# Kernel optimization log

Measured on AMD Instinct MI355X. Metric: run time of the kernel, lower is better.

## Reference

```python
import jax, jax.numpy as jnp
import numpy as np

B, C, H, W = 8, 128, 64, 64
D_STATE = 16
D_CONV = 4
EXPAND = 1.25
D_INNER = int(EXPAND * C)        # 160
DT_RANK = int(np.ceil(C / 16))   # 8


def setup_inputs() -> dict:
    key = jax.random.key(0)
    ks = jax.random.split(key, 10)
    f = lambda k, s, sc=0.02: jax.random.normal(k, s, dtype=jnp.float32) * sc
    return {
        "x": jax.random.normal(ks[0], (B, C, H, W), dtype=jnp.float32),
        "ln_g": jnp.ones((C,), jnp.float32),
        "ln_b": jnp.zeros((C,), jnp.float32),
        "in_proj_w": f(ks[1], (2 * D_INNER, C)),
        "conv_w": f(ks[2], (D_INNER, 1, D_CONV)),            # depthwise causal conv kernel
        "conv_b": jnp.zeros((D_INNER,), jnp.float32),
        "x_proj_w": f(ks[3], (DT_RANK + 2 * D_STATE, D_INNER)),
        "dt_proj_w": f(ks[4], (D_INNER, DT_RANK), 0.1),
        "dt_proj_b": f(ks[5], (D_INNER,), 0.1),
        # S4-style init: A_log = log(1..d_state) per inner channel (frozen in torch module)
        "A_log": jnp.log(jnp.tile(jnp.arange(1, D_STATE + 1, dtype=jnp.float32), (D_INNER, 1))),
        "D_param": jnp.ones((D_INNER,), jnp.float32),
        "out_proj_w": f(ks[6], (C, D_INNER)),
        "fuse_w": f(ks[7], (C, 2 * C)),                      # 1x1 conv == per-token matmul
        "scale": jnp.ones((1,), jnp.float32) * 0.1,
    }


def _layernorm(x, g, b, eps=1e-5):
    m = x.mean(-1, keepdims=True)
    v = x.var(-1, keepdims=True)
    return (x - m) * jax.lax.rsqrt(v + eps) * g + b


def _mamba(seq, in_proj_w, conv_w, conv_b, x_proj_w, dt_proj_w, dt_proj_b,
           A_log, D_param, out_proj_w):
    # seq: (B, L, C)
    Bsz, L, _ = seq.shape
    xz = jnp.einsum('blc,ec->ble', seq, in_proj_w)           # (B, L, 2*d_inner)
    xm, z = jnp.split(xz, 2, axis=-1)
    # depthwise causal conv over L, truncated to L (padding = d_conv-1 on the left)
    xc = jax.lax.conv_general_dilated(
        xm.transpose(0, 2, 1), conv_w, (1,), [(D_CONV - 1, 0)],
        feature_group_count=D_INNER, dimension_numbers=('NCH', 'OIH', 'NCH'))
    xm = jax.nn.silu((xc + conv_b[None, :, None]).transpose(0, 2, 1))  # (B, L, d_inner)
    x_dbl = jnp.einsum('bld,ed->ble', xm, x_proj_w)
    dt = x_dbl[..., :DT_RANK]
    Bm = x_dbl[..., DT_RANK:DT_RANK + D_STATE]               # (B, L, d_state)
    Cm = x_dbl[..., DT_RANK + D_STATE:]                      # (B, L, d_state)
    dt = jax.nn.softplus(jnp.einsum('blr,dr->bld', dt, dt_proj_w) + dt_proj_b)
    A = -jnp.exp(A_log)                                      # (d_inner, d_state)

    def step(h, inp):
        dt_t, B_t, C_t, x_t = inp                            # (B,d) (B,n) (B,n) (B,d)
        dA = jnp.exp(dt_t[:, :, None] * A)                   # (B, d_inner, d_state)
        h = dA * h + (dt_t * x_t)[:, :, None] * B_t[:, None, :]
        y = jnp.einsum('bdn,bn->bd', h, C_t)
        return h, y

    h0 = jnp.zeros((Bsz, D_INNER, D_STATE), dtype=seq.dtype)
    xs = (dt.transpose(1, 0, 2), Bm.transpose(1, 0, 2),
          Cm.transpose(1, 0, 2), xm.transpose(1, 0, 2))
    _, ys = jax.lax.scan(step, h0, xs)                       # ys: (L, B, d_inner)
    y = ys.transpose(1, 0, 2) + xm * D_param
    y = y * jax.nn.silu(z)
    return jnp.einsum('bld,cd->blc', y, out_proj_w)          # (B, L, C)


def reference(x, ln_g, ln_b, in_proj_w, conv_w, conv_b, x_proj_w, dt_proj_w,
              dt_proj_b, A_log, D_param, out_proj_w, fuse_w, scale):
    Bsz, Ch, Hh, Ww = x.shape
    seq = x.reshape(Bsz, Ch, Hh * Ww).transpose(0, 2, 1)     # (B, L, C) raster order
    seq_n = _layernorm(seq, ln_g, ln_b)                      # LN is per-token: commutes with flip
    args = (in_proj_w, conv_w, conv_b, x_proj_w, dt_proj_w, dt_proj_b,
            A_log, D_param, out_proj_w)
    y0 = _mamba(seq_n, *args)                                # forward raster scan
    y1 = _mamba(seq_n[:, ::-1, :], *args)[:, ::-1, :]        # reversed raster scan
    fused = jnp.einsum('blk,ck->blc', jnp.concatenate([y0, y1], axis=-1), fuse_w)
    out = seq + scale * fused                                # residual + learned scale
    return out.transpose(0, 2, 1).reshape(Bsz, Ch, Hh, Ww)
```

## Files before the change

kernel.cpp:

```cpp
#include <hip/hip_runtime.h>
#include <math.h>

#define LSEQ   4096
#define BATCH  8
#define CDIM   128
#define DIN    160
#define DSTATE 16
#define DTRANK 8
#define BLROWS (BATCH*LSEQ)
#define NCHUNK 256
#define TCH    16
#define SUBC   16
#define NSEG   16

typedef __attribute__((ext_vector_type(8))) short short8;
typedef __attribute__((ext_vector_type(8))) __bf16 bf16x8;
typedef __attribute__((ext_vector_type(4))) float float4v;

__device__ __forceinline__ float4v mfma_bf16(short8 a, short8 b, float4v c) {
  return __builtin_amdgcn_mfma_f32_16x16x32_bf16(
      __builtin_bit_cast(bf16x8, a), __builtin_bit_cast(bf16x8, b), c, 0, 0, 0);
}

__device__ __forceinline__ unsigned short f2bf(float f) {
  union { float f; unsigned u; } v; v.f = f;
  unsigned r = v.u + 0x7FFF + ((v.u >> 16) & 1);
  return (unsigned short)(r >> 16);
}
__device__ __forceinline__ float bf2f(unsigned short h) {
  union { unsigned u; float f; } v; v.u = ((unsigned)h) << 16;
  return v.f;
}

__global__ void prep_weights(const float* __restrict__ inpw, const float* __restrict__ xpw,
                             const float* __restrict__ fuse_w, const float* __restrict__ out_proj_w,
                             unsigned short* __restrict__ inpw_bf, unsigned short* __restrict__ xpw_bf,
                             unsigned short* __restrict__ W01) {
  int i = blockIdx.x * 256 + threadIdx.x;
  if (i < 320 * 128) inpw_bf[i] = f2bf(inpw[i]);
  if (i < 40 * 160)  xpw_bf[i]  = f2bf(xpw[i]);
  if (i < CDIM * DIN) {
    int d = i % DIN, c = i / DIN;
    float a0 = 0.f, a1 = 0.f;
    for (int k = 0; k < CDIM; ++k) {
      float o = out_proj_w[k * DIN + d];
      a0 += fuse_w[c * 256 + k] * o;
      a1 += fuse_w[c * 256 + 128 + k] * o;
    }
    W01[c * DIN + d] = f2bf(a0);
    W01[CDIM * DIN + c * DIN + d] = f2bf(a1);
  }
}

__global__ void ln_transpose_kernel(const float* __restrict__ x,
                                    const float* __restrict__ g,
                                    const float* __restrict__ bb,
                                    unsigned short* __restrict__ seqn) {
  __shared__ float sA[128 * 65];
  __shared__ float psum[2 * 256];
  __shared__ float mrs[2 * 64];
  int l0 = blockIdx.x * 64;
  int b  = blockIdx.y;
  int t  = threadIdx.x;
  int lsub = t & 63, crow = t >> 6;
  const float* xb = x + (size_t)b * CDIM * LSEQ;
  for (int it = 0; it < 32; ++it) {
    int c = crow + it * 4;
    sA[c * 65 + lsub] = xb[(size_t)c * LSEQ + l0 + lsub];
  }
  __syncthreads();
  float s = 0.f, ss = 0.f;
  for (int j = 0; j < 32; ++j) {
    int c = crow * 32 + j;
    float v = sA[c * 65 + lsub];
    s += v; ss += v * v;
  }
  psum[crow * 64 + lsub] = s;
  psum[256 + crow * 64 + lsub] = ss;
  __syncthreads();
  if (t < 64) {
    float su = 0.f, sq = 0.f;
    for (int p = 0; p < 4; ++p) { su += psum[p * 64 + t]; sq += psum[256 + p * 64 + t]; }
    float m = su * (1.f / 128.f);
    float var = sq * (1.f / 128.f) - m * m;
    mrs[t] = m;
    mrs[64 + t] = rsqrtf(var + 1e-5f);
  }
  __syncthreads();
  int c = t & 127, half = t >> 7;
  float gc = g[c], bc = bb[c];
  for (int it = 0; it < 32; ++it) {
    int l = it * 2 + half;
    float v = (sA[c * 65 + l] - mrs[l]) * mrs[64 + l] * gc + bc;
    seqn[((size_t)(b * LSEQ + l0 + l)) * CDIM + c] = f2bf(v);
  }
}

template<int K, bool MASKN, bool BF16OUT>
__global__ __launch_bounds__(256)
void gemm_mfma(const unsigned short* __restrict__ A0, const unsigned short* __restrict__ A1,
               const unsigned short* __restrict__ W,
               void* __restrict__ C0, void* __restrict__ C1, int N) {
  constexpr int LSTR = K + 8;
  __shared__ __align__(16) unsigned short As[64 * LSTR];
  __shared__ __align__(16) unsigned short Ws[64 * LSTR];
  const unsigned short* A = blockIdx.z ? A1 : A0;
  void* Cp = blockIdx.z ? C1 : C0;
  int m0 = blockIdx.x * 64;
  int n0 = blockIdx.y * 64;
  int t = threadIdx.x;
  constexpr int CH = 64 * K / 8;
  for (int c = t; c < CH; c += 256) {
    int row = c / (K / 8);
    int col = (c % (K / 8)) * 8;
    *(short8*)&As[row * LSTR + col] = *(const short8*)&A[(size_t)(m0 + row) * K + col];
    short8 wv = {};
    int nr = n0 + row;
    if (!MASKN || nr < N) wv = *(const short8*)&W[(size_t)nr * K + col];
    *(short8*)&Ws[row * LSTR + col] = wv;
  }
  __syncthreads();
  int lane = t & 63;
  int w = t >> 6;
  int l15 = lane & 15, quad = lane >> 4;
  float4v acc[4] = {};
#pragma unroll
  for (int kk = 0; kk < K; kk += 32) {
    short8 bfrag = *(const short8*)&Ws[(w * 16 + l15) * LSTR + kk + quad * 8];
#pragma unroll
    for (int i = 0; i < 4; ++i) {
      short8 afrag = *(const short8*)&As[(i * 16 + l15) * LSTR + kk + quad * 8];
      acc[i] = mfma_bf16(afrag, bfrag, acc[i]);
    }
  }
  int col = n0 + w * 16 + l15;
  if (MASKN && col >= N) return;
#pragma unroll
  for (int i = 0; i < 4; ++i)
#pragma unroll
    for (int r = 0; r < 4; ++r) {
      int row = m0 + i * 16 + quad * 4 + r;
      if (BF16OUT) ((unsigned short*)Cp)[(size_t)row * N + col] = f2bf(acc[i][r]);
      else         ((float*)Cp)[(size_t)row * N + col] = acc[i][r];
    }
}

__global__ void conv_silu_kernel(const unsigned short* __restrict__ xz,
                                 const float* __restrict__ cw,
                                 const float* __restrict__ cb,
                                 unsigned short* __restrict__ xm0,
                                 unsigned short* __restrict__ xm1,
                                 _Float16* __restrict__ szp) {
  int idx = blockIdx.x * 256 + threadIdx.x;
  int dir = blockIdx.y;
  if (idx >= BLROWS * 80) return;
  int dp = idx % 80;
  int bl = idx / 80;
  int l = bl % LSEQ, b = bl / LSEQ;
  int d = dp * 2;
  float w0[4], w1[4];
#pragma unroll
  for (int k = 0; k < 4; ++k) { w0[k] = cw[d * 4 + k]; w1[k] = cw[d * 4 + 4 + k]; }
  float a0 = cb[d], a1 = cb[d + 1];
  const unsigned short* base = xz + ((size_t)b * LSEQ) * 320 + d;
  if (dir == 0) {
#pragma unroll
    for (int k = 0; k < 4; ++k) {
      int lp = l - 3 + k;
      if (lp >= 0) {
        unsigned v = *(const unsigned*)&base[(size_t)lp * 320];
        a0 += w0[k] * bf2f((unsigned short)v);
        a1 += w1[k] * bf2f((unsigned short)(v >> 16));
      }
    }
  } else {
#pragma unroll
    for (int k = 0; k < 4; ++k) {
      int lp = l + 3 - k;
      if (lp < LSEQ) {
        unsigned v = *(const unsigned*)&base[(size_t)lp * 320];
        a0 += w0[k] * bf2f((unsigned short)v);
        a1 += w1[k] * bf2f((unsigned short)(v >> 16));
      }
    }
  }
  float s0 = a0 / (1.f + __expf(-a0));
  float s1 = a1 / (1.f + __expf(-a1));
  unsigned outv = (unsigned)f2bf(s0) | ((unsigned)f2bf(s1) << 16);
  unsigned short* xm = dir ? xm1 : xm0;
  *(unsigned*)&xm[(size_t)bl * DIN + d] = outv;
  if (dir == 0) {
    unsigned zv = *(const unsigned*)&xz[(size_t)bl * 320 + 160 + d];
    float z0 = bf2f((unsigned short)zv), z1 = bf2f((unsigned short)(zv >> 16));
    float g0 = z0 / (1.f + __expf(-z0));
    float g1 = z1 / (1.f + __expf(-z1));
    unsigned short h0 = __builtin_bit_cast(unsigned short, (_Float16)g0);
    unsigned short h1 = __builtin_bit_cast(unsigned short, (_Float16)g1);
    *(unsigned*)&szp[(size_t)bl * DIN + d] = (unsigned)h0 | ((unsigned)h1 << 16);
  }
}

__device__ __forceinline__ void decay_powers(float r1, float* dA) {
  float r2 = r1 * r1;
  float r4 = r2 * r2;
  float r8 = r4 * r4;
  dA[0] = r1;       dA[1] = r2;       dA[2] = r2 * r1;  dA[3] = r4;
  dA[4] = r4 * r1;  dA[5] = r4 * r2;  dA[6] = r4 * dA[2]; dA[7] = r8;
  dA[8] = r8 * r1;  dA[9] = r8 * r2;  dA[10] = r8 * dA[2]; dA[11] = r8 * r4;
  dA[12] = r8 * dA[4]; dA[13] = r8 * dA[5]; dA[14] = r8 * dA[6]; dA[15] = r8 * r8;
}

__global__ __launch_bounds__(192, 6)
void scan_passA(const float* __restrict__ xdbl0, const float* __restrict__ xdbl1,
                const unsigned short* __restrict__ xm0v, const unsigned short* __restrict__ xm1v,
                const float* __restrict__ dt_w, const float* __restrict__ dt_b,
                const float* __restrict__ Dp,
                float* __restrict__ Q, float* __restrict__ dtsum,
                unsigned* __restrict__ yr0, unsigned* __restrict__ yr1) {
  __shared__ __align__(16) float sx[TCH * 40];
  __shared__ __align__(16) unsigned short sxm[TCH * DIN];
  int chunk = blockIdx.x, b = blockIdx.y, dir = blockIdx.z;
  int t = threadIdx.x;
  const float* xdbl = dir ? xdbl1 : xdbl0;
  const unsigned short* xm = dir ? xm1v : xm0v;
  unsigned* yr = dir ? yr1 : yr0;
  int l00 = dir ? (LSEQ - 1 - chunk * TCH) : (chunk * TCH);
  int step = dir ? -1 : 1;
  int rowbase = b * LSEQ + l00;
  for (int i = t; i < TCH * 40; i += 192) {
    int tt = i / 40, j = i - tt * 40;
    sx[i] = xdbl[(size_t)(rowbase + step * tt) * 40 + j];
  }
  for (int i = t; i < TCH * (DIN / 2); i += 192) {
    int tt = i / 80, j = i - tt * 80;
    ((unsigned*)sxm)[i] = *(const unsigned*)&xm[(size_t)(rowbase + step * tt) * DIN + 2 * j];
  }
  __syncthreads();
  if (t >= DIN) return;
  int d = t;
  float dw[8];
#pragma unroll
  for (int r = 0; r < 8; ++r) dw[r] = dt_w[d * 8 + r];
  float db = dt_b[d];
  float Dd = Dp[d];
  float h[16];
#pragma unroll
  for (int n = 0; n < 16; ++n) h[n] = 0.f;
  float cum = 0.f;
  float rcum = 1.f;
  unsigned* yrp = yr + (size_t)rowbase * DIN + d;
#pragma unroll 4
  for (int tt = 0; tt < TCH; ++tt) {
    const float* xrow = &sx[tt * 40];
    float xmv = bf2f(sxm[tt * DIN + d]);
    float zz = db;
#pragma unroll
    for (int r = 0; r < 8; ++r) zz += xrow[r] * dw[r];
    float e  = __expf(fminf(zz, 20.f));
    float dt = (zz > 20.f) ? zz : __logf(1.f + e);
    float r1 = 1.f / (1.f + e);
    cum += dt;
    rcum *= r1;
    float u = dt * xmv;
    float dA[16];
    decay_powers(r1, dA);
    float y = xmv * Dd;
#pragma unroll
    for (int n = 0; n < 16; ++n) {
      h[n] = dA[n] * h[n] + u * xrow[8 + n];
      y += h[n] * xrow[24 + n];
    }
    unsigned short rch = __builtin_bit_cast(unsigned short, (_Float16)rcum);
    *yrp = (unsigned)f2bf(y) | ((unsigned)rch << 16);
    yrp += step * DIN;
  }
  size_t base = (size_t)((dir * BATCH + b) * NCHUNK + chunk);
#pragma unroll
  for (int n = 0; n < 16; ++n) Q[base * (DIN * 16) + d * 16 + n] = h[n];
  dtsum[base * DIN + d] = cum;
}

__global__ __launch_bounds__(256)
void scan_passB(const float* Q, const float* __restrict__ dtsum,
                float* Hinit) {
  __shared__ float sA[NSEG * 16], sQ[NSEG * 16];
  int blk = blockIdx.x;
  int d = blk % DIN;
  int rem = blk / DIN;
  int t = threadIdx.x;
  int n = t & 15, cs = t >> 4;
  float An = -(float)(n + 1);
  float a[SUBC], q[SUBC];
  float Aseg = 1.f, Qseg = 0.f;
#pragma unroll
  for (int j = 0; j < SUBC; ++j) {
    int ch = cs * SUBC + j;
    size_t base = (size_t)rem * NCHUNK + ch;
    float dsv = dtsum[base * DIN + d];
    float av = __expf(An * dsv);
    float qv = Q[base * (DIN * 16) + d * 16 + n];
    a[j] = av; q[j] = qv;
    Qseg = av * Qseg + qv;
    Aseg *= av;
  }
  sA[cs * 16 + n] = Aseg;
  sQ[cs * 16 + n] = Qseg;
  __syncthreads();
  if (t < 16) {
    float h = 0.f;
    for (int s = 0; s < NSEG; ++s) {
      float Av = sA[s * 16 + t], Qv = sQ[s * 16 + t];
      sA[s * 16 + t] = h;
      h = Av * h + Qv;
    }
  }
  __syncthreads();
  float h = sA[cs * 16 + n];
#pragma unroll
  for (int j = 0; j < SUBC; ++j) {
    int ch = cs * SUBC + j;
    size_t base = (size_t)rem * NCHUNK + ch;
    Hinit[base * (DIN * 16) + d * 16 + n] = h;
    h = a[j] * h + q[j];
  }
}

__global__ __launch_bounds__(192, 6)
void scan_passC(const float* __restrict__ xdbl0, const float* __restrict__ xdbl1,
                const _Float16* __restrict__ szp,
                const float* __restrict__ Hinit,
                const unsigned* __restrict__ yr0, const unsigned* __restrict__ yr1,
                unsigned short* __restrict__ yg0, unsigned short* __restrict__ yg1) {
  __shared__ __align__(16) float sC[TCH * 16];
  __shared__ __align__(16) unsigned syr[TCH * DIN];
  __shared__ __align__(16) _Float16 ssz[TCH * DIN];
  int chunk = blockIdx.x, b = blockIdx.y, dir = blockIdx.z;
  int t = threadIdx.x;
  const float* xdbl = dir ? xdbl1 : xdbl0;
  const unsigned* yrb = dir ? yr1 : yr0;
  unsigned short* yg = dir ? yg1 : yg0;
  int l00 = dir ? (LSEQ - 1 - chunk * TCH) : (chunk * TCH);
  int step = dir ? -1 : 1;
  int rowbase = b * LSEQ + l00;
  for (int i = t; i < TCH * 16; i += 192) {
    int tt = i >> 4, j = i & 15;
    sC[i] = xdbl[(size_t)(rowbase + step * tt) * 40 + 24 + j];
  }
  for (int i = t; i < TCH * DIN; i += 192) {
    int tt = i / DIN, j = i - tt * DIN;
    syr[i] = yrb[(size_t)(rowbase + step * tt) * DIN + j];
  }
  for (int i = t; i < TCH * (DIN / 2); i += 192) {
    int tt = i / 80, j = i - tt * 80;
    ((unsigned*)ssz)[i] = *(const unsigned*)&szp[(size_t)(rowbase + step * tt) * DIN + 2 * j];
  }
  __syncthreads();
  if (t >= DIN) return;
  int d = t;
  size_t base = (size_t)((dir * BATCH + b) * NCHUNK + chunk);
  float H0[16];
#pragma unroll
  for (int n = 0; n < 16; ++n) H0[n] = Hinit[base * (DIN * 16) + d * 16 + n];
  unsigned short* ygp = yg + (size_t)rowbase * DIN + d;
#pragma unroll 4
  for (int tt = 0; tt < TCH; ++tt) {
    unsigned v = syr[tt * DIN + d];
    float y = bf2f((unsigned short)v);
    float rcum = (float)__builtin_bit_cast(_Float16, (unsigned short)(v >> 16));
    float sz = (float)ssz[tt * DIN + d];
    const float* cr = &sC[tt * 16];
    float dA[16];
    decay_powers(rcum, dA);
    float corr = 0.f;
#pragma unroll
    for (int n = 0; n < 16; ++n) corr += cr[n] * (dA[n] * H0[n]);
    *ygp = f2bf((y + corr) * sz);
    ygp += step * DIN;
  }
}

__global__ __launch_bounds__(256)
void final_mfma(const unsigned short* __restrict__ yg0, const unsigned short* __restrict__ yg1,
                const unsigned short* __restrict__ W01, const float* __restrict__ x,
                const float* __restrict__ scale, float* __restrict__ out) {
  constexpr int K = DIN, LSTR = K + 8;
  __shared__ __align__(16) unsigned short As[64 * LSTR];
  __shared__ __align__(16) unsigned short Ws[64 * LSTR];
  float* sC = (float*)As;
  int m0 = blockIdx.x * 64;
  int c0 = blockIdx.y * 64;
  int b = m0 / LSEQ, l0 = m0 % LSEQ;
  int t = threadIdx.x;
  int lane = t & 63;
  int w = t >> 6;
  int l15 = lane & 15, quad = lane >> 4;
  float4v acc[4] = {};
  for (int pass = 0; pass < 2; ++pass) {
    const unsigned short* A = pass ? yg1 : yg0;
    const unsigned short* W = W01 + pass * (CDIM * K);
    if (pass) __syncthreads();
    constexpr int CH = 64 * K / 8;
    for (int c = t; c < CH; c += 256) {
      int row = c / (K / 8);
      int col = (c % (K / 8)) * 8;
      *(short8*)&As[row * LSTR + col] = *(const short8*)&A[(size_t)(m0 + row) * K + col];
      *(short8*)&Ws[row * LSTR + col] = *(const short8*)&W[(size_t)(c0 + row) * K + col];
    }
    __syncthreads();
#pragma unroll
    for (int kk = 0; kk < K; kk += 32) {
      short8 bfrag = *(const short8*)&Ws[(w * 16 + l15) * LSTR + kk + quad * 8];
#pragma unroll
      for (int i = 0; i < 4; ++i) {
        short8 afrag = *(const short8*)&As[(i * 16 + l15) * LSTR + kk + quad * 8];
        acc[i] = mfma_bf16(afrag, bfrag, acc[i]);
      }
    }
  }
  __syncthreads();
#pragma unroll
  for (int i = 0; i < 4; ++i)
#pragma unroll
    for (int r = 0; r < 4; ++r)
      sC[(i * 16 + quad * 4 + r) * 65 + w * 16 + l15] = acc[i][r];
  __syncthreads();
  float sc = scale[0];
  int ll = t & 63, cq = t >> 6;
#pragma unroll
  for (int j = 0; j < 16; ++j) {
    int cl = cq * 16 + j;
    float v = sC[ll * 65 + cl];
    size_t gi = ((size_t)(b * CDIM + c0 + cl)) * LSEQ + l0 + ll;
    out[gi] = x[gi] + sc * v;
  }
}

extern "C" void kernel_launch(void* const* d_in, const int* in_sizes, int n_in,
                              void* d_out, int out_size, void* d_ws, size_t ws_size,
                              hipStream_t stream) {
  const float* x        = (const float*)d_in[0];
  const float* ln_g     = (const float*)d_in[1];
  const float* ln_b     = (const float*)d_in[2];
  const float* in_projw = (const float*)d_in[3];
  const float* conv_w   = (const float*)d_in[4];
  const float* conv_b   = (const float*)d_in[5];
  const float* x_projw  = (const float*)d_in[6];
  const float* dt_projw = (const float*)d_in[7];
  const float* dt_projb = (const float*)d_in[8];
  const float* A_log    = (const float*)d_in[9];
  const float* D_param  = (const float*)d_in[10];
  const float* out_projw= (const float*)d_in[11];
  const float* fuse_w   = (const float*)d_in[12];
  const float* scale    = (const float*)d_in[13];
  float* out = (float*)d_out;
  (void)A_log;

  float* ws = (float*)d_ws;
  size_t off = 0;
  unsigned short* seqn_bf = (unsigned short*)(ws + off); off += (size_t)BLROWS * CDIM / 2;
  unsigned short* xz      = (unsigned short*)(ws + off); off += (size_t)BLROWS * 320 / 2;
  unsigned short* xm0 = (unsigned short*)(ws + off); off += (size_t)BLROWS * DIN / 2;
  unsigned short* xm1 = (unsigned short*)(ws + off); off += (size_t)BLROWS * DIN / 2;
  float* xdbl0 = ws + off; off += (size_t)BLROWS * 40;
  float* xdbl1 = ws + off; off += (size_t)BLROWS * 40;
  float* Q     = ws + off; off += (size_t)2 * BATCH * NCHUNK * DIN * 16;
  float* Hinit = Q;
  float* dtsum = ws + off; off += (size_t)2 * BATCH * NCHUNK * DIN;
  unsigned* yr0 = (unsigned*)(ws + off); off += (size_t)BLROWS * DIN;
  unsigned* yr1 = (unsigned*)(ws + off); off += (size_t)BLROWS * DIN;
  unsigned short* yg0 = (unsigned short*)(ws + off); off += (size_t)BLROWS * DIN / 2;
  unsigned short* yg1 = (unsigned short*)(ws + off); off += (size_t)BLROWS * DIN / 2;
  _Float16* szv = (_Float16*)(ws + off); off += (size_t)BLROWS * DIN / 2;
  unsigned short* W01bf = (unsigned short*)(ws + off); off += (size_t)2 * CDIM * DIN / 2;
  unsigned short* inpw_bf = (unsigned short*)(ws + off); off += (size_t)320 * 128 / 2;
  unsigned short* xpw_bf  = (unsigned short*)(ws + off); off += (size_t)40 * 160 / 2 + 8;

  prep_weights<<<(320 * 128 + 255) / 256, 256, 0, stream>>>(
      in_projw, x_projw, fuse_w, out_projw, inpw_bf, xpw_bf, W01bf);
  ln_transpose_kernel<<<dim3(LSEQ / 64, BATCH), 256, 0, stream>>>(x, ln_g, ln_b, seqn_bf);
  gemm_mfma<128, false, true><<<dim3(BLROWS / 64, 5, 1), 256, 0, stream>>>(
      seqn_bf, seqn_bf, inpw_bf, xz, xz, 320);
  conv_silu_kernel<<<dim3((BLROWS * 80 + 255) / 256, 2), 256, 0, stream>>>(
      xz, conv_w, conv_b, xm0, xm1, szv);
  gemm_mfma<160, true, false><<<dim3(BLROWS / 64, 1, 2), 256, 0, stream>>>(
      xm0, xm1, xpw_bf, xdbl0, xdbl1, 40);
  scan_passA<<<dim3(NCHUNK, BATCH, 2), 192, 0, stream>>>(xdbl0, xdbl1, xm0, xm1,
                                                         dt_projw, dt_projb, D_param,
                                                         Q, dtsum, yr0, yr1);
  scan_passB<<<2 * BATCH * DIN, 256, 0, stream>>>(Q, dtsum, Hinit);
  scan_passC<<<dim3(NCHUNK, BATCH, 2), 192, 0, stream>>>(xdbl0, xdbl1, szv, Hinit,
                                                         yr0, yr1, yg0, yg1);
  final_mfma<<<dim3(BLROWS / 64, CDIM / 64), 256, 0, stream>>>(yg0, yg1, W01bf, x, scale, out);
}
```

Before: 267.0 us.

## Drop LDS staging in scan passes, read rows via scalar loads, double chunk length

Scan passes A and C no longer stage chunk data in shared memory behind a block barrier. Each thread now reads the per-token x_dbl row through a wave-uniform (readfirstlane) pointer, which lets the compiler use scalar loads, and reads its xm/yr/sz values straight from global memory. The chunk length doubles to 32 with half as many chunks, which halves the cross-chunk state traffic and the pass-B work but lengthens the serial dependency per thread. The change also splits the reductions into independent accumulators, vectorizes the Q and Hinit accesses, and replaces divisions with hardware reciprocals, at a small cost in accuracy.

```diff
diff --git a/kernel.cpp b/kernel.cpp
--- a/kernel.cpp
+++ b/kernel.cpp
@@ -8,9 +8,9 @@
 #define DSTATE 16
 #define DTRANK 8
 #define BLROWS (BATCH*LSEQ)
-#define NCHUNK 256
-#define TCH    16
-#define SUBC   16
+#define NCHUNK 128
+#define TCH    32
+#define SUBC   8
 #define NSEG   16
 
 typedef __attribute__((ext_vector_type(8))) short short8;
@@ -184,16 +184,16 @@
       }
     }
   }
-  float s0 = a0 / (1.f + __expf(-a0));
-  float s1 = a1 / (1.f + __expf(-a1));
+  float s0 = a0 * __builtin_amdgcn_rcpf(1.f + __expf(-a0));
+  float s1 = a1 * __builtin_amdgcn_rcpf(1.f + __expf(-a1));
   unsigned outv = (unsigned)f2bf(s0) | ((unsigned)f2bf(s1) << 16);
   unsigned short* xm = dir ? xm1 : xm0;
   *(unsigned*)&xm[(size_t)bl * DIN + d] = outv;
   if (dir == 0) {
     unsigned zv = *(const unsigned*)&xz[(size_t)bl * 320 + 160 + d];
     float z0 = bf2f((unsigned short)zv), z1 = bf2f((unsigned short)(zv >> 16));
-    float g0 = z0 / (1.f + __expf(-z0));
-    float g1 = z1 / (1.f + __expf(-z1));
+    float g0 = z0 * __builtin_amdgcn_rcpf(1.f + __expf(-z0));
+    float g1 = z1 * __builtin_amdgcn_rcpf(1.f + __expf(-z1));
     unsigned short h0 = __builtin_bit_cast(unsigned short, (_Float16)g0);
     unsigned short h1 = __builtin_bit_cast(unsigned short, (_Float16)g1);
     *(unsigned*)&szp[(size_t)bl * DIN + d] = (unsigned)h0 | ((unsigned)h1 << 16);
@@ -210,33 +210,22 @@
   dA[12] = r8 * dA[4]; dA[13] = r8 * dA[5]; dA[14] = r8 * dA[6]; dA[15] = r8 * r8;
 }
 
-__global__ __launch_bounds__(192, 6)
-void scan_passA(const float* __restrict__ xdbl0, const float* __restrict__ xdbl1,
-                const unsigned short* __restrict__ xm0v, const unsigned short* __restrict__ xm1v,
-                const float* __restrict__ dt_w, const float* __restrict__ dt_b,
-                const float* __restrict__ Dp,
-                float* __restrict__ Q, float* __restrict__ dtsum,
-                unsigned* __restrict__ yr0, unsigned* __restrict__ yr1) {
-  __shared__ __align__(16) float sx[TCH * 40];
-  __shared__ __align__(16) unsigned short sxm[TCH * DIN];
+__device__ __forceinline__ const float* uniform_row(const float* base, int elem_off) {
+  return base + __builtin_amdgcn_readfirstlane(elem_off);
+}
+
+__global__ void scan_passA(const float* __restrict__ xdbl0, const float* __restrict__ xdbl1,
+                           const unsigned short* __restrict__ xm0v, const unsigned short* __restrict__ xm1v,
+                           const float* __restrict__ dt_w, const float* __restrict__ dt_b,
+                           const float* __restrict__ Dp,
+                           float* __restrict__ Q, float* __restrict__ dtsum,
+                           unsigned* __restrict__ yr0, unsigned* __restrict__ yr1) {
   int chunk = blockIdx.x, b = blockIdx.y, dir = blockIdx.z;
   int t = threadIdx.x;
+  if (t >= DIN) return;
   const float* xdbl = dir ? xdbl1 : xdbl0;
   const unsigned short* xm = dir ? xm1v : xm0v;
   unsigned* yr = dir ? yr1 : yr0;
-  int l00 = dir ? (LSEQ - 1 - chunk * TCH) : (chunk * TCH);
-  int step = dir ? -1 : 1;
-  int rowbase = b * LSEQ + l00;
-  for (int i = t; i < TCH * 40; i += 192) {
-    int tt = i / 40, j = i - tt * 40;
-    sx[i] = xdbl[(size_t)(rowbase + step * tt) * 40 + j];
-  }
-  for (int i = t; i < TCH * (DIN / 2); i += 192) {
-    int tt = i / 80, j = i - tt * 80;
-    ((unsigned*)sxm)[i] = *(const unsigned*)&xm[(size_t)(rowbase + step * tt) * DIN + 2 * j];
-  }
-  __syncthreads();
-  if (t >= DIN) return;
   int d = t;
   float dw[8];
 #pragma unroll
@@ -248,35 +237,49 @@
   for (int n = 0; n < 16; ++n) h[n] = 0.f;
   float cum = 0.f;
   float rcum = 1.f;
+  int l00 = dir ? (LSEQ - 1 - chunk * TCH) : (chunk * TCH);
+  int step = dir ? -1 : 1;
+  int rowbase = b * LSEQ + l00;
   unsigned* yrp = yr + (size_t)rowbase * DIN + d;
 #pragma unroll 4
   for (int tt = 0; tt < TCH; ++tt) {
-    const float* xrow = &sx[tt * 40];
-    float xmv = bf2f(sxm[tt * DIN + d]);
-    float zz = db;
-#pragma unroll
-    for (int r = 0; r < 8; ++r) zz += xrow[r] * dw[r];
+    int rowi = rowbase + step * tt;
+    const float* xr = uniform_row(xdbl, rowi * 40);
+    float xmv = bf2f(xm[(size_t)rowi * DIN + d]);
+    float za = db, zb = 0.f;
+#pragma unroll
+    for (int r = 0; r < 8; r += 2) { za += xr[r] * dw[r]; zb += xr[r + 1] * dw[r + 1]; }
+    float zz = za + zb;
     float e  = __expf(fminf(zz, 20.f));
     float dt = (zz > 20.f) ? zz : __logf(1.f + e);
-    float r1 = 1.f / (1.f + e);
+    float r1 = __builtin_amdgcn_rcpf(1.f + e);
     cum += dt;
     rcum *= r1;
     float u = dt * xmv;
     float dA[16];
     decay_powers(r1, dA);
-    float y = xmv * Dd;
-#pragma unroll
-    for (int n = 0; n < 16; ++n) {
-      h[n] = dA[n] * h[n] + u * xrow[8 + n];
-      y += h[n] * xrow[24 + n];
-    }
+#pragma unroll
+    for (int n = 0; n < 16; ++n) h[n] = dA[n] * h[n] + u * xr[8 + n];
+    float y0 = xmv * Dd, y1 = 0.f, y2 = 0.f, y3 = 0.f;
+#pragma unroll
+    for (int n = 0; n < 4; ++n) {
+      y0 += h[n]      * xr[24 + n];
+      y1 += h[4 + n]  * xr[28 + n];
+      y2 += h[8 + n]  * xr[32 + n];
+      y3 += h[12 + n] * xr[36 + n];
+    }
+    float y = (y0 + y1) + (y2 + y3);
     unsigned short rch = __builtin_bit_cast(unsigned short, (_Float16)rcum);
     *yrp = (unsigned)f2bf(y) | ((unsigned)rch << 16);
     yrp += step * DIN;
   }
   size_t base = (size_t)((dir * BATCH + b) * NCHUNK + chunk);
-#pragma unroll
-  for (int n = 0; n < 16; ++n) Q[base * (DIN * 16) + d * 16 + n] = h[n];
+  float4v* qp = (float4v*)&Q[base * (DIN * 16) + d * 16];
+#pragma unroll
+  for (int n = 0; n < 4; ++n) {
+    float4v qv = { h[4 * n], h[4 * n + 1], h[4 * n + 2], h[4 * n + 3] };
+    qp[n] = qv;
+  }
   dtsum[base * DIN + d] = cum;
 }
 
@@ -325,55 +328,50 @@
   }
 }
 
-__global__ __launch_bounds__(192, 6)
-void scan_passC(const float* __restrict__ xdbl0, const float* __restrict__ xdbl1,
-                const _Float16* __restrict__ szp,
-                const float* __restrict__ Hinit,
-                const unsigned* __restrict__ yr0, const unsigned* __restrict__ yr1,
-                unsigned short* __restrict__ yg0, unsigned short* __restrict__ yg1) {
-  __shared__ __align__(16) float sC[TCH * 16];
-  __shared__ __align__(16) unsigned syr[TCH * DIN];
-  __shared__ __align__(16) _Float16 ssz[TCH * DIN];
+__global__ void scan_passC(const float* __restrict__ xdbl0, const float* __restrict__ xdbl1,
+                           const _Float16* __restrict__ szp,
+                           const float* __restrict__ Hinit,
+                           const unsigned* __restrict__ yr0, const unsigned* __restrict__ yr1,
+                           unsigned short* __restrict__ yg0, unsigned short* __restrict__ yg1) {
   int chunk = blockIdx.x, b = blockIdx.y, dir = blockIdx.z;
   int t = threadIdx.x;
+  if (t >= DIN) return;
   const float* xdbl = dir ? xdbl1 : xdbl0;
   const unsigned* yrb = dir ? yr1 : yr0;
   unsigned short* yg = dir ? yg1 : yg0;
+  int d = t;
+  size_t base = (size_t)((dir * BATCH + b) * NCHUNK + chunk);
+  float H0[16];
+  const float4v* hp = (const float4v*)&Hinit[base * (DIN * 16) + d * 16];
+#pragma unroll
+  for (int n = 0; n < 4; ++n) {
+    float4v hv = hp[n];
+    H0[4 * n] = hv[0]; H0[4 * n + 1] = hv[1]; H0[4 * n + 2] = hv[2]; H0[4 * n + 3] = hv[3];
+  }
   int l00 = dir ? (LSEQ - 1 - chunk * TCH) : (chunk * TCH);
   int step = dir ? -1 : 1;
   int rowbase = b * LSEQ + l00;
-  for (int i = t; i < TCH * 16; i += 192) {
-    int tt = i >> 4, j = i & 15;
-    sC[i] = xdbl[(size_t)(rowbase + step * tt) * 40 + 24 + j];
-  }
-  for (int i = t; i < TCH * DIN; i += 192) {
-    int tt = i / DIN, j = i - tt * DIN;
-    syr[i] = yrb[(size_t)(rowbase + step * tt) * DIN + j];
-  }
-  for (int i = t; i < TCH * (DIN / 2); i += 192) {
-    int tt = i / 80, j = i - tt * 80;
-    ((unsigned*)ssz)[i] = *(const unsigned*)&szp[(size_t)(rowbase + step * tt) * DIN + 2 * j];
-  }
-  __syncthreads();
-  if (t >= DIN) return;
-  int d = t;
-  size_t base = (size_t)((dir * BATCH + b) * NCHUNK + chunk);
-  float H0[16];
-#pragma unroll
-  for (int n = 0; n < 16; ++n) H0[n] = Hinit[base * (DIN * 16) + d * 16 + n];
   unsigned short* ygp = yg + (size_t)rowbase * DIN + d;
-#pragma unroll 4
+#pragma unroll 2
   for (int tt = 0; tt < TCH; ++tt) {
-    unsigned v = syr[tt * DIN + d];
+    int rowi = rowbase + step * tt;
+    const float* xr = uniform_row(xdbl, rowi * 40 + 24);
+    size_t di = (size_t)rowi * DIN + d;
+    unsigned v = yrb[di];
     float y = bf2f((unsigned short)v);
     float rcum = (float)__builtin_bit_cast(_Float16, (unsigned short)(v >> 16));
-    float sz = (float)ssz[tt * DIN + d];
-    const float* cr = &sC[tt * 16];
+    float sz = (float)szp[di];
     float dA[16];
     decay_powers(rcum, dA);
-    float corr = 0.f;
-#pragma unroll
-    for (int n = 0; n < 16; ++n) corr += cr[n] * (dA[n] * H0[n]);
+    float c0 = 0.f, c1 = 0.f, c2 = 0.f, c3 = 0.f;
+#pragma unroll
+    for (int n = 0; n < 4; ++n) {
+      c0 += xr[n]      * (dA[n]      * H0[n]);
+      c1 += xr[4 + n]  * (dA[4 + n]  * H0[4 + n]);
+      c2 += xr[8 + n]  * (dA[8 + n]  * H0[8 + n]);
+      c3 += xr[12 + n] * (dA[12 + n] * H0[12 + n]);
+    }
+    float corr = (c0 + c1) + (c2 + c3);
     *ygp = f2bf((y + corr) * sz);
     ygp += step * DIN;
   }
```

Result: faster. 248.0 us (-7.1%).
